# Kernel optimization log

Measured on AMD Instinct MI355X. Metric: run time of the kernel, lower is better.

The kernel has to match this reference:

```python
import jax, jax.numpy as jnp
import numpy as np

N = 50000      # nodes (src = dst at both layers)
E = 800000     # edges per layer
T = 8          # time steps
C_IN = 16      # input channels
HID = 16       # conv1 out channels (hardcoded in SAGENet)
C_OUT = 32     # final out channels


def setup_inputs() -> dict:
    key = jax.random.key(0)
    ks = jax.random.split(key, 10)
    X = jax.random.normal(ks[0], (T, N, C_IN), dtype=jnp.float32)
    edge_index0 = jax.random.randint(ks[1], (2, E), 0, N, dtype=jnp.int32)
    edge_weight0 = jax.random.uniform(ks[2], (E,), dtype=jnp.float32)
    edge_index1 = jax.random.randint(ks[3], (2, E), 0, N, dtype=jnp.int32)
    edge_weight1 = jax.random.uniform(ks[4], (E,), dtype=jnp.float32)
    res_n_id0 = jnp.arange(N, dtype=jnp.int32)
    res_n_id1 = jnp.arange(N, dtype=jnp.int32)
    W1 = jax.random.normal(ks[5], (2 * C_IN, HID), dtype=jnp.float32) * 0.1
    b1 = jax.random.normal(ks[6], (HID,), dtype=jnp.float32) * 0.1
    W2 = jax.random.normal(ks[7], (2 * HID, C_OUT), dtype=jnp.float32) * 0.1
    b2 = jax.random.normal(ks[8], (C_OUT,), dtype=jnp.float32) * 0.1
    return {"X": X, "edge_index0": edge_index0, "edge_weight0": edge_weight0,
            "edge_index1": edge_index1, "edge_weight1": edge_weight1,
            "res_n_id0": res_n_id0, "res_n_id1": res_n_id1,
            "W1": W1, "b1": b1, "W2": W2, "b2": b2}


def sage_conv(x, edge_index, edge_weight, res_n_id, num_dst, W, b):
    # x: [N_src, T, C]; message = edge_weight * x[src]; mean-aggregate to dst;
    # concat residual x[res_n_id] then linear (old PyG SAGEConv, concat=True).
    src, dst = edge_index[0], edge_index[1]
    msg = x[src] * edge_weight[:, None, None]                      # [E, T, C]
    summed = jax.ops.segment_sum(msg, dst, num_segments=num_dst)   # [Nd, T, C]
    cnt = jax.ops.segment_sum(jnp.ones_like(edge_weight), dst, num_segments=num_dst)
    aggr = summed / jnp.maximum(cnt, 1.0)[:, None, None]
    h = jnp.concatenate([x[res_n_id], aggr], axis=-1)              # [Nd, T, 2C]
    return jnp.einsum('ntc,cd->ntd', h, W) + b


def reference(X, edge_index0, edge_weight0, edge_index1, edge_weight1,
              res_n_id0, res_n_id1, W1, b1, W2, b2):
    x = jnp.transpose(X, (1, 0, 2))                                # [N, T, C]
    x = jax.nn.leaky_relu(sage_conv(x, edge_index0, edge_weight0, res_n_id0, N, W1, b1), 0.01)
    x = jax.nn.leaky_relu(sage_conv(x, edge_index1, edge_weight1, res_n_id1, N, W2, b2), 0.01)
    return jnp.transpose(x, (1, 0, 2))                             # [T, N, C_out]
```

## Files before the change

kernel.cpp:

```cpp
#include <hip/hip_runtime.h>
#include <hip/hip_bf16.h>
#include <stdint.h>

static constexpr int Nn   = 50000;
static constexpr int Ee   = 800000;
static constexpr int Tt   = 8;
static constexpr int CIN  = 16;
static constexpr int HID  = 16;
static constexpr int COUT = 32;
static constexpr int TC   = Tt * CIN;
static constexpr int ROWD = TC / 2;

static constexpr int NB  = (2 * Nn + 255) / 256;
static constexpr int CAP = 16;
static constexpr int GSTR = 32;

static constexpr int BINB = 768;
static constexpr int EPB  = (2 * Ee + BINB - 1) / BINB;
static constexpr int TRB  = 1536;

typedef __attribute__((ext_vector_type(8))) short short8;
typedef __attribute__((ext_vector_type(4))) float f32x4;
union FU { uint4 u4; short8 s8; };

__device__ inline float bflo(uint32_t u) { return __uint_as_float(u << 16); }
__device__ inline float bfhi(uint32_t u) { return __uint_as_float(u & 0xffff0000u); }
__device__ inline unsigned short f2bf(float x) {
    __hip_bfloat16 h = __float2bfloat16(x);
    unsigned short u; __builtin_memcpy(&u, &h, 2); return u;
}
__device__ inline uint32_t bfpack(float a, float b) {
    return (uint32_t)f2bf(a) | ((uint32_t)f2bf(b) << 16);
}
__device__ inline void redg(float2& a) {
    a.x += __shfl_xor(a.x, 16); a.y += __shfl_xor(a.y, 16);
    a.x += __shfl_xor(a.x, 32); a.y += __shfl_xor(a.y, 32);
}

__device__ inline float dot2bf(float acc, uint32_t w2, uint32_t x2) {
    asm("v_dot2_f32_bf16 %0, %1, %2, %0" : "+v"(acc) : "v"(w2), "v"(x2));
    return acc;
}
__device__ inline void dotp(float2& a0, float2& a1, float2& a2, float2& a3,
                            uint32_t w2, uint4 r0, uint4 r1) {
    uint32_t lo, hi;
    lo = __builtin_amdgcn_perm(r1.x, r0.x, 0x05040100u);
    hi = __builtin_amdgcn_perm(r1.x, r0.x, 0x07060302u);
    a0.x = dot2bf(a0.x, w2, lo);
    a0.y = dot2bf(a0.y, w2, hi);
    lo = __builtin_amdgcn_perm(r1.y, r0.y, 0x05040100u);
    hi = __builtin_amdgcn_perm(r1.y, r0.y, 0x07060302u);
    a1.x = dot2bf(a1.x, w2, lo);
    a1.y = dot2bf(a1.y, w2, hi);
    lo = __builtin_amdgcn_perm(r1.z, r0.z, 0x05040100u);
    hi = __builtin_amdgcn_perm(r1.z, r0.z, 0x07060302u);
    a2.x = dot2bf(a2.x, w2, lo);
    a2.y = dot2bf(a2.y, w2, hi);
    lo = __builtin_amdgcn_perm(r1.w, r0.w, 0x05040100u);
    hi = __builtin_amdgcn_perm(r1.w, r0.w, 0x07060302u);
    a3.x = dot2bf(a3.x, w2, lo);
    a3.y = dot2bf(a3.y, w2, hi);
}

__global__ __launch_bounds__(256) void k_count_detect(
        const int* __restrict__ ei0, const int* __restrict__ ei1,
        int* __restrict__ bucketCnt,
        const unsigned short* __restrict__ x16, int nvals,
        int* __restrict__ flag,
        const void* W1, const void* b1, const void* W2, const void* b2,
        float* __restrict__ biasbuf,
        uint32_t* __restrict__ wpk1, uint32_t* __restrict__ wpk2) {
    int tid = threadIdx.x;
    if (blockIdx.x >= 256) {
        __shared__ int bad;
        if (tid == 0) bad = 0;
        __syncthreads();
        for (int i = tid; i < nvals; i += 256) {
            int ex = (x16[i] >> 7) & 0xFF;
            if (ex >= 0x8D) atomicOr(&bad, 1);
        }
        __syncthreads();
        int f = bad;
        if (tid == 0) flag[0] = f;
        auto ldf = [&](const void* srcp, int idx) -> float {
            return f ? ((const float*)srcp)[idx]
                     : __bfloat162float(((const __hip_bfloat16*)srcp)[idx]);
        };
        if (tid < 16) biasbuf[tid] = ldf(b1, tid);
        if (tid >= 16 && tid < 48) biasbuf[tid] = ldf(b2, tid - 16);
        { int h = tid >> 4, d = tid & 15;
          wpk1[tid] = bfpack(ldf(W1, 2 * d * 16 + h), ldf(W1, (2 * d + 1) * 16 + h)); }
        for (int i = tid; i < 512; i += 256) {
            int h = i >> 4, d = i & 15;
            wpk2[i] = bfpack(ldf(W2, 2 * d * 32 + h), ldf(W2, (2 * d + 1) * 32 + h));
        }
        return;
    }
    __shared__ int hist[NB];
    for (int i = tid; i < NB; i += 256) hist[i] = 0;
    __syncthreads();
    const int4* d0 = (const int4*)(ei0 + Ee);
    const int4* d1 = (const int4*)(ei1 + Ee);
    int stride = 256 * 256;
    int nq = Ee / 4;
    for (int i = blockIdx.x * 256 + tid; i < 2 * nq; i += stride) {
        int4 v; int addn;
        if (i < nq) { v = d0[i]; addn = 0; }
        else        { v = d1[i - nq]; addn = Nn; }
        atomicAdd(&hist[(v.x + addn) >> 8], 1);
        atomicAdd(&hist[(v.y + addn) >> 8], 1);
        atomicAdd(&hist[(v.z + addn) >> 8], 1);
        atomicAdd(&hist[(v.w + addn) >> 8], 1);
    }
    __syncthreads();
    for (int i = tid; i < NB; i += 256)
        if (hist[i]) atomicAdd(&bucketCnt[i], hist[i]);
}

__global__ void k_bucketscan(const int* __restrict__ bucketCnt,
                             int* __restrict__ base, int* __restrict__ gcur) {
    __shared__ int tmp[512];
    int tid = threadIdx.x;
    int v = (tid < NB) ? bucketCnt[tid] : 0;
    tmp[tid] = v;
    __syncthreads();
    for (int ofs = 1; ofs < 512; ofs <<= 1) {
        int t = (tid >= ofs) ? tmp[tid - ofs] : 0;
        __syncthreads();
        tmp[tid] += t;
        __syncthreads();
    }
    if (tid < NB) {
        int b = tmp[tid] - v;
        base[tid] = b;
        gcur[tid * GSTR] = b;
    }
    if (tid == 0) base[NB] = 2 * Ee;
}

__global__ __launch_bounds__(256) void k_bin_tr(const int* __restrict__ flag,
        const int* __restrict__ ei0, const void* w0v,
        const int* __restrict__ ei1, const void* w1v,
        int* __restrict__ gcur, uint64_t* __restrict__ gout,
        const void* Xv, uint32_t* __restrict__ xrows) {
    __shared__ uint64_t rows[NB][CAP];
    __shared__ int cnt[NB];
    __shared__ int posArr[NB];
    int tid = threadIdx.x;
    int bid = blockIdx.x;
    if (bid >= BINB) {
        int f = flag[0];
        int stride = TRB * 256;
        for (int i = (bid - BINB) * 256 + tid; i < Nn * ROWD; i += stride) {
            int n = i >> 6;
            int l = i & 63;
            int t = l >> 3;
            int c = (l & 7) * 2;
            int sidx = (t * Nn + n) * CIN + c;
            uint32_t v;
            if (f) {
                float2 ab = ((const float2*)Xv)[sidx >> 1];
                v = bfpack(ab.x, ab.y);
            } else {
                const unsigned short* u = (const unsigned short*)Xv;
                v = (uint32_t)u[sidx] | ((uint32_t)u[sidx + 1] << 16);
            }
            xrows[i] = v;
        }
        return;
    }
    for (int i = tid; i < NB; i += 256) cnt[i] = 0;
    __syncthreads();
    int f = flag[0];
    int lo = bid * EPB;
    int hi = min(2 * Ee, lo + EPB);
    for (int e = lo + tid; e < hi; e += 256) {
        int g; uint32_t src, wb;
        if (e < Ee) {
            g = ei0[Ee + e];
            src = (uint32_t)ei0[e];
            wb = f ? f2bf(((const float*)w0v)[e])
                   : ((const unsigned short*)w0v)[e];
        } else {
            int e1 = e - Ee;
            g = Nn + ei1[Ee + e1];
            src = (uint32_t)ei1[e1];
            wb = f ? f2bf(((const float*)w1v)[e1])
                   : ((const unsigned short*)w1v)[e1];
        }
        uint64_t r = ((uint64_t)(uint32_t)g << 32) | (src << 16) | wb;
        int b = g >> 8;
        int idx = atomicAdd(&cnt[b], 1);
        if (idx < CAP) rows[b][idx ^ (b & (CAP - 1))] = r;
        else { int pos = atomicAdd(&gcur[b * GSTR], 1); gout[pos] = r; }
    }
    __syncthreads();
    for (int b = tid; b < NB; b += 256) {
        int c = min(cnt[b], CAP);
        posArr[b] = c ? atomicAdd(&gcur[b * GSTR], c) : 0;
    }
    __syncthreads();
    int wv = tid >> 6, lane = tid & 63;
    int q = lane >> 4, k = lane & 15;
    for (int b = wv * 4 + q; b < NB; b += 16) {
        int c = min(cnt[b], CAP);
        if (k < c) gout[posArr[b] + k] = rows[b][k ^ (b & (CAP - 1))];
    }
}

__global__ __launch_bounds__(256) void k_csr(const int* __restrict__ base,
        const uint64_t* __restrict__ gout,
        int* __restrict__ off, uint32_t* __restrict__ rec) {
    __shared__ int hist[256];
    __shared__ int tmp[256];
    __shared__ int cur[256];
    __shared__ uint32_t stage[8192];
    int b = blockIdx.x, tid = threadIdx.x;
    int lo = base[b], hi = base[b + 1];
    hist[tid] = 0;
    __syncthreads();
    for (int i = lo + tid; i < hi; i += 256) {
        int gl = (int)(gout[i] >> 32) & 255;
        atomicAdd(&hist[gl], 1);
    }
    __syncthreads();
    int v = hist[tid];
    tmp[tid] = v;
    __syncthreads();
    for (int ofs = 1; ofs < 256; ofs <<= 1) {
        int t = (tid >= ofs) ? tmp[tid - ofs] : 0;
        __syncthreads();
        tmp[tid] += t;
        __syncthreads();
    }
    int excl = tmp[tid] - v;
    int gg = (b << 8) + tid;
    if (gg < 2 * Nn) off[gg] = lo + excl;
    if (b == NB - 1 && tid == 0) off[2 * Nn] = 2 * Ee;
    int count = hi - lo;
    if (count <= 8192) {
        cur[tid] = excl;
        __syncthreads();
        for (int i = lo + tid; i < hi; i += 256) {
            uint64_t r = gout[i];
            int gl = (int)(r >> 32) & 255;
            int pos = atomicAdd(&cur[gl], 1);
            stage[pos] = (uint32_t)r;
        }
        __syncthreads();
        for (int i = tid; i < count; i += 256) rec[lo + i] = stage[i];
    } else {
        cur[tid] = lo + excl;
        __syncthreads();
        for (int i = lo + tid; i < hi; i += 256) {
            uint64_t r = gout[i];
            int gl = (int)(r >> 32) & 255;
            int pos = atomicAdd(&cur[gl], 1);
            rec[pos] = (uint32_t)r;
        }
    }
}


__global__ __launch_bounds__(256) void k_layer1(
    const uint32_t* __restrict__ xrows, const int* __restrict__ off,
    const uint32_t* __restrict__ rec, const int* __restrict__ resid,
    const uint32_t* __restrict__ wpk1, const float* __restrict__ biasbuf,
    uint32_t* __restrict__ h1rows) {
    __shared__ __align__(16) uint32_t shA[32 * 20];
    int tid = threadIdx.x, wv = tid >> 6, lane = tid & 63;
    int g = lane >> 4, p = lane & 15;
    uint4 bfr = ((const uint4*)wpk1)[p * 4 + g];
    float bias = biasbuf[p];
    int n = blockIdx.x * 4 + wv;
    int o0 = __builtin_amdgcn_readfirstlane(off[n]);
    int o1 = __builtin_amdgcn_readfirstlane(off[n + 1]);
    int rn = __builtin_amdgcn_readfirstlane(resid[n]);
    const uint4* xb = (const uint4*)xrows;
    uint4 xs4 = xb[rn * 16 + p];
    float2 a0 = {0.f, 0.f}, a1 = a0, a2 = a0, a3 = a0;
    for (int j = o0; j < o1; j += 16) {
        int j0 = j + g, j1 = j + 4 + g, j2 = j + 8 + g, j3 = j + 12 + g;
        uint32_t e0 = rec[min(j0, o1 - 1)];
        uint32_t e1 = rec[min(j1, o1 - 1)];
        uint32_t e2 = rec[min(j2, o1 - 1)];
        uint32_t e3 = rec[min(j3, o1 - 1)];
        uint4 r0 = xb[(int)(e0 >> 16) * 16 + p];
        uint4 r1 = xb[(int)(e1 >> 16) * 16 + p];
        uint4 r2 = xb[(int)(e2 >> 16) * 16 + p];
        uint4 r3 = xb[(int)(e3 >> 16) * 16 + p];
        uint32_t w0 = (j0 < o1) ? (e0 & 0xffffu) : 0u;
        uint32_t w1 = (j1 < o1) ? (e1 & 0xffffu) : 0u;
        uint32_t w2 = (j2 < o1) ? (e2 & 0xffffu) : 0u;
        uint32_t w3 = (j3 < o1) ? (e3 & 0xffffu) : 0u;
        uint32_t wA = w0 | (w1 << 16);
        uint32_t wB = w2 | (w3 << 16);
        dotp(a0, a1, a2, a3, wA, r0, r1);
        dotp(a0, a1, a2, a3, wB, r2, r3);
    }
    redg(a0); redg(a1); redg(a2); redg(a3);
    float inv = 1.f / (float)max(o1 - o0, 1);
    uint4 agp;
    agp.x = bfpack(a0.x * inv, a0.y * inv);
    agp.y = bfpack(a1.x * inv, a1.y * inv);
    agp.z = bfpack(a2.x * inv, a2.y * inv);
    agp.w = bfpack(a3.x * inv, a3.y * inv);
    int r = wv * 8 + (p >> 1);
    int hs = (p & 1) * 4;
    if (g == 0)      *(uint4*)&shA[r * 20 + hs] = xs4;
    else if (g == 1) *(uint4*)&shA[r * 20 + 8 + hs] = agp;
    __syncthreads();
    FU fa, fb; fb.u4 = bfr;
    fa.u4 = *(const uint4*)&shA[((wv >> 1) * 16 + p) * 20 + 4 * g];
    f32x4 acc = {bias, bias, bias, bias};
    acc = __builtin_amdgcn_mfma_f32_16x16x32_bf16(fa.s8, fb.s8, acc, 0, 0, 0);
    bool mine = ((g >> 1) == (wv & 1));
#pragma unroll
    for (int rg = 0; rg < 4; rg++) {
        float v = acc[rg];
        v = fmaxf(v, 0.01f * v);
        float vn = __shfl_xor(v, 1);
        if (mine && !(p & 1)) {
            int t = (g & 1) * 4 + rg;
            h1rows[n * 64 + t * 8 + (p >> 1)] = bfpack(v, vn);
        }
    }
}

__global__ __launch_bounds__(256) void k_layer2(
    const int* __restrict__ flag,
    const uint32_t* __restrict__ h1rows, const int* __restrict__ off,
    const uint32_t* __restrict__ rec, const int* __restrict__ resid,
    const uint32_t* __restrict__ wpk2, const float* __restrict__ biasbuf,
    void* __restrict__ outv) {
    __shared__ __align__(16) uint32_t shA[32 * 20];
    int tid = threadIdx.x, wv = tid >> 6, lane = tid & 63;
    int g = lane >> 4, p = lane & 15;
    uint4 b0 = ((const uint4*)wpk2)[p * 4 + g];
    uint4 b1v = ((const uint4*)wpk2)[(p + 16) * 4 + g];
    float bias0 = biasbuf[16 + p];
    float bias1 = biasbuf[32 + p];
    int f = flag[0];
    int n = blockIdx.x * 4 + wv;
    int o0 = __builtin_amdgcn_readfirstlane(off[Nn + n]);
    int o1 = __builtin_amdgcn_readfirstlane(off[Nn + n + 1]);
    int rn = __builtin_amdgcn_readfirstlane(resid[n]);
    const uint4* xb = (const uint4*)h1rows;
    uint4 xs4 = xb[rn * 16 + p];
    float2 a0 = {0.f, 0.f}, a1 = a0, a2 = a0, a3 = a0;
    for (int j = o0; j < o1; j += 16) {
        int j0 = j + g, j1 = j + 4 + g, j2 = j + 8 + g, j3 = j + 12 + g;
        uint32_t e0 = rec[min(j0, o1 - 1)];
        uint32_t e1 = rec[min(j1, o1 - 1)];
        uint32_t e2 = rec[min(j2, o1 - 1)];
        uint32_t e3 = rec[min(j3, o1 - 1)];
        uint4 r0 = xb[(int)(e0 >> 16) * 16 + p];
        uint4 r1 = xb[(int)(e1 >> 16) * 16 + p];
        uint4 r2 = xb[(int)(e2 >> 16) * 16 + p];
        uint4 r3 = xb[(int)(e3 >> 16) * 16 + p];
        uint32_t w0 = (j0 < o1) ? (e0 & 0xffffu) : 0u;
        uint32_t w1 = (j1 < o1) ? (e1 & 0xffffu) : 0u;
        uint32_t w2 = (j2 < o1) ? (e2 & 0xffffu) : 0u;
        uint32_t w3 = (j3 < o1) ? (e3 & 0xffffu) : 0u;
        uint32_t wA = w0 | (w1 << 16);
        uint32_t wB = w2 | (w3 << 16);
        dotp(a0, a1, a2, a3, wA, r0, r1);
        dotp(a0, a1, a2, a3, wB, r2, r3);
    }
    redg(a0); redg(a1); redg(a2); redg(a3);
    float inv = 1.f / (float)max(o1 - o0, 1);
    uint4 agp;
    agp.x = bfpack(a0.x * inv, a0.y * inv);
    agp.y = bfpack(a1.x * inv, a1.y * inv);
    agp.z = bfpack(a2.x * inv, a2.y * inv);
    agp.w = bfpack(a3.x * inv, a3.y * inv);
    int r = wv * 8 + (p >> 1);
    int hs = (p & 1) * 4;
    if (g == 0)      *(uint4*)&shA[r * 20 + hs] = xs4;
    else if (g == 1) *(uint4*)&shA[r * 20 + 8 + hs] = agp;
    __syncthreads();
    FU fa, fb0, fb1; fb0.u4 = b0; fb1.u4 = b1v;
    fa.u4 = *(const uint4*)&shA[((wv >> 1) * 16 + p) * 20 + 4 * g];
    f32x4 acc0 = {bias0, bias0, bias0, bias0};
    f32x4 acc1 = {bias1, bias1, bias1, bias1};
    acc0 = __builtin_amdgcn_mfma_f32_16x16x32_bf16(fa.s8, fb0.s8, acc0, 0, 0, 0);
    acc1 = __builtin_amdgcn_mfma_f32_16x16x32_bf16(fa.s8, fb1.s8, acc1, 0, 0, 0);
    bool mine = ((g >> 1) == (wv & 1));
    if (mine) {
#pragma unroll
        for (int rg = 0; rg < 4; rg++) {
            int t = (g & 1) * 4 + rg;
            size_t idx = ((size_t)(t * Nn + n)) * COUT + p;
            float v = acc0[rg]; v = fmaxf(v, 0.01f * v);
            float u = acc1[rg]; u = fmaxf(u, 0.01f * u);
            if (f) {
                ((float*)outv)[idx] = v;
                ((float*)outv)[idx + 16] = u;
            } else {
                ((__hip_bfloat16*)outv)[idx] = __float2bfloat16(v);
                ((__hip_bfloat16*)outv)[idx + 16] = __float2bfloat16(u);
            }
        }
    }
}


extern "C" void kernel_launch(void* const* d_in, const int* in_sizes, int n_in,
                              void* d_out, int out_size, void* d_ws, size_t ws_size,
                              hipStream_t stream) {
    const void* X   = d_in[0];
    const int* ei0  = (const int*)d_in[1];
    const void* w0  = d_in[2];
    const int* ei1  = (const int*)d_in[3];
    const void* w1  = d_in[4];
    const int* rn0  = (const int*)d_in[5];
    const int* rn1  = (const int*)d_in[6];
    const void* W1  = d_in[7];
    const void* b1  = d_in[8];
    const void* W2  = d_in[9];
    const void* b2  = d_in[10];

    char* ws = (char*)d_ws;
    size_t p = 0;
    auto alloc = [&](size_t bytes) -> char* {
        p = (p + 255) & ~(size_t)255;
        char* r = ws + p;
        p += bytes;
        return r;
    };
    int* flag        = (int*)alloc(4);
    float* biasbuf   = (float*)alloc(48 * 4);
    uint32_t* wpk1   = (uint32_t*)alloc(256 * 4);
    uint32_t* wpk2   = (uint32_t*)alloc(512 * 4);
    int* bucketCnt   = (int*)alloc(NB * 4);
    int* base        = (int*)alloc((NB + 1) * 4);
    int* gcur        = (int*)alloc((size_t)NB * GSTR * 4);
    int* off         = (int*)alloc(((size_t)2 * Nn + 1) * 4);
    uint32_t* recf   = (uint32_t*)alloc((size_t)2 * Ee * 4);
    uint32_t* h1rows = (uint32_t*)alloc((size_t)Nn * ROWD * 4);
    uint64_t* gout   = (uint64_t*)alloc((size_t)2 * Ee * 8);
    uint32_t* xrows  = (uint32_t*)d_out;

    hipMemsetAsync(bucketCnt, 0, NB * sizeof(int), stream);
    hipLaunchKernelGGL(k_count_detect, dim3(257), dim3(256), 0, stream,
                       ei0, ei1, bucketCnt,
                       (const unsigned short*)X, 16384, flag, W1, b1, W2, b2,
                       biasbuf, wpk1, wpk2);
    hipLaunchKernelGGL(k_bucketscan, dim3(1), dim3(512), 0, stream,
                       bucketCnt, base, gcur);
    hipLaunchKernelGGL(k_bin_tr, dim3(BINB + TRB), dim3(256), 0, stream,
                       flag, ei0, w0, ei1, w1, gcur, gout, X, xrows);
    hipLaunchKernelGGL(k_csr, dim3(NB), dim3(256), 0, stream,
                       base, gout, off, recf);
    hipLaunchKernelGGL(k_layer1, dim3(Nn / 4), dim3(256), 0, stream,
                       xrows, off, recf, rn0, wpk1, biasbuf, h1rows);
    hipLaunchKernelGGL(k_layer2, dim3(Nn / 4), dim3(256), 0, stream,
                       flag, h1rows, off, recf, rn1, wpk2, biasbuf, d_out);
    (void)in_sizes; (void)n_in; (void)out_size; (void)ws_size;
}
```

Measured before the change: 245.9 us.

## Process two destination nodes per wavefront in both layer kernels

Each wavefront now aggregates two destination nodes at once, interleaving their gathers with 8 edges per iteration per node instead of 16 for one. This lets every wave fill a full 16-row MFMA tile, so all lanes store results and the grid is halved. The bf16 output path in layer 2 now packs pairs with shuffles into 32-bit stores. In exchange, the loop runs to the larger of the two degrees, which can waste lanes when degrees differ, and register pressure rises.

```diff
diff --git a/kernel.cpp b/kernel.cpp
--- a/kernel.cpp
+++ b/kernel.cpp
@@ -23,8 +23,6 @@
 typedef __attribute__((ext_vector_type(4))) float f32x4;
 union FU { uint4 u4; short8 s8; };
 
-__device__ inline float bflo(uint32_t u) { return __uint_as_float(u << 16); }
-__device__ inline float bfhi(uint32_t u) { return __uint_as_float(u & 0xffff0000u); }
 __device__ inline unsigned short f2bf(float x) {
     __hip_bfloat16 h = __float2bfloat16(x);
     unsigned short u; __builtin_memcpy(&u, &h, 2); return u;
@@ -267,61 +265,74 @@
     const uint32_t* __restrict__ rec, const int* __restrict__ resid,
     const uint32_t* __restrict__ wpk1, const float* __restrict__ biasbuf,
     uint32_t* __restrict__ h1rows) {
-    __shared__ __align__(16) uint32_t shA[32 * 20];
+    __shared__ __align__(16) uint32_t shA[64 * 20];
     int tid = threadIdx.x, wv = tid >> 6, lane = tid & 63;
     int g = lane >> 4, p = lane & 15;
     uint4 bfr = ((const uint4*)wpk1)[p * 4 + g];
     float bias = biasbuf[p];
-    int n = blockIdx.x * 4 + wv;
-    int o0 = __builtin_amdgcn_readfirstlane(off[n]);
-    int o1 = __builtin_amdgcn_readfirstlane(off[n + 1]);
-    int rn = __builtin_amdgcn_readfirstlane(resid[n]);
+    int n0 = blockIdx.x * 8 + wv * 2;
+    int oA0 = __builtin_amdgcn_readfirstlane(off[n0]);
+    int oM  = __builtin_amdgcn_readfirstlane(off[n0 + 1]);
+    int oB1 = __builtin_amdgcn_readfirstlane(off[n0 + 2]);
+    int rnA = __builtin_amdgcn_readfirstlane(resid[n0]);
+    int rnB = __builtin_amdgcn_readfirstlane(resid[n0 + 1]);
+    int cA = oM - oA0, cB = oB1 - oM;
+    int lastA = max(oM - 1, 0), lastB = max(oB1 - 1, 0);
     const uint4* xb = (const uint4*)xrows;
-    uint4 xs4 = xb[rn * 16 + p];
-    float2 a0 = {0.f, 0.f}, a1 = a0, a2 = a0, a3 = a0;
-    for (int j = o0; j < o1; j += 16) {
-        int j0 = j + g, j1 = j + 4 + g, j2 = j + 8 + g, j3 = j + 12 + g;
-        uint32_t e0 = rec[min(j0, o1 - 1)];
-        uint32_t e1 = rec[min(j1, o1 - 1)];
-        uint32_t e2 = rec[min(j2, o1 - 1)];
-        uint32_t e3 = rec[min(j3, o1 - 1)];
-        uint4 r0 = xb[(int)(e0 >> 16) * 16 + p];
-        uint4 r1 = xb[(int)(e1 >> 16) * 16 + p];
-        uint4 r2 = xb[(int)(e2 >> 16) * 16 + p];
-        uint4 r3 = xb[(int)(e3 >> 16) * 16 + p];
-        uint32_t w0 = (j0 < o1) ? (e0 & 0xffffu) : 0u;
-        uint32_t w1 = (j1 < o1) ? (e1 & 0xffffu) : 0u;
-        uint32_t w2 = (j2 < o1) ? (e2 & 0xffffu) : 0u;
-        uint32_t w3 = (j3 < o1) ? (e3 & 0xffffu) : 0u;
-        uint32_t wA = w0 | (w1 << 16);
-        uint32_t wB = w2 | (w3 << 16);
-        dotp(a0, a1, a2, a3, wA, r0, r1);
-        dotp(a0, a1, a2, a3, wB, r2, r3);
-    }
-    redg(a0); redg(a1); redg(a2); redg(a3);
-    float inv = 1.f / (float)max(o1 - o0, 1);
-    uint4 agp;
-    agp.x = bfpack(a0.x * inv, a0.y * inv);
-    agp.y = bfpack(a1.x * inv, a1.y * inv);
-    agp.z = bfpack(a2.x * inv, a2.y * inv);
-    agp.w = bfpack(a3.x * inv, a3.y * inv);
-    int r = wv * 8 + (p >> 1);
+    uint4 xsA = xb[rnA * 16 + p];
+    uint4 xsB = xb[rnB * 16 + p];
+    float2 aA0 = {0.f, 0.f}, aA1 = aA0, aA2 = aA0, aA3 = aA0;
+    float2 aB0 = aA0, aB1 = aA0, aB2 = aA0, aB3 = aA0;
+    int cmax = max(cA, cB);
+    for (int j = 0; j < cmax; j += 8) {
+        int j0 = j + g, j1 = j + 4 + g;
+        uint32_t eA0 = rec[min(oA0 + j0, lastA)];
+        uint32_t eA1 = rec[min(oA0 + j1, lastA)];
+        uint32_t eB0 = rec[min(oM + j0, lastB)];
+        uint32_t eB1 = rec[min(oM + j1, lastB)];
+        uint4 rA0 = xb[(int)(eA0 >> 16) * 16 + p];
+        uint4 rA1 = xb[(int)(eA1 >> 16) * 16 + p];
+        uint4 rB0 = xb[(int)(eB0 >> 16) * 16 + p];
+        uint4 rB1 = xb[(int)(eB1 >> 16) * 16 + p];
+        uint32_t wA = ((j0 < cA) ? (eA0 & 0xffffu) : 0u)
+                    | (((j1 < cA) ? (eA1 & 0xffffu) : 0u) << 16);
+        uint32_t wB = ((j0 < cB) ? (eB0 & 0xffffu) : 0u)
+                    | (((j1 < cB) ? (eB1 & 0xffffu) : 0u) << 16);
+        dotp(aA0, aA1, aA2, aA3, wA, rA0, rA1);
+        dotp(aB0, aB1, aB2, aB3, wB, rB0, rB1);
+    }
+    redg(aA0); redg(aA1); redg(aA2); redg(aA3);
+    redg(aB0); redg(aB1); redg(aB2); redg(aB3);
+    float invA = 1.f / (float)max(cA, 1);
+    float invB = 1.f / (float)max(cB, 1);
+    uint4 agpA, agpB;
+    agpA.x = bfpack(aA0.x * invA, aA0.y * invA);
+    agpA.y = bfpack(aA1.x * invA, aA1.y * invA);
+    agpA.z = bfpack(aA2.x * invA, aA2.y * invA);
+    agpA.w = bfpack(aA3.x * invA, aA3.y * invA);
+    agpB.x = bfpack(aB0.x * invB, aB0.y * invB);
+    agpB.y = bfpack(aB1.x * invB, aB1.y * invB);
+    agpB.z = bfpack(aB2.x * invB, aB2.y * invB);
+    agpB.w = bfpack(aB3.x * invB, aB3.y * invB);
+    int rA = wv * 16 + (p >> 1);
     int hs = (p & 1) * 4;
-    if (g == 0)      *(uint4*)&shA[r * 20 + hs] = xs4;
-    else if (g == 1) *(uint4*)&shA[r * 20 + 8 + hs] = agp;
+    if (g == 0)      *(uint4*)&shA[rA * 20 + hs] = xsA;
+    else if (g == 1) *(uint4*)&shA[rA * 20 + 8 + hs] = agpA;
+    else if (g == 2) *(uint4*)&shA[(rA + 8) * 20 + hs] = xsB;
+    else             *(uint4*)&shA[(rA + 8) * 20 + 8 + hs] = agpB;
     __syncthreads();
     FU fa, fb; fb.u4 = bfr;
-    fa.u4 = *(const uint4*)&shA[((wv >> 1) * 16 + p) * 20 + 4 * g];
+    fa.u4 = *(const uint4*)&shA[(wv * 16 + p) * 20 + 4 * g];
     f32x4 acc = {bias, bias, bias, bias};
     acc = __builtin_amdgcn_mfma_f32_16x16x32_bf16(fa.s8, fb.s8, acc, 0, 0, 0);
-    bool mine = ((g >> 1) == (wv & 1));
 #pragma unroll
     for (int rg = 0; rg < 4; rg++) {
         float v = acc[rg];
         v = fmaxf(v, 0.01f * v);
         float vn = __shfl_xor(v, 1);
-        if (mine && !(p & 1)) {
+        if (!(p & 1)) {
             int t = (g & 1) * 4 + rg;
+            int n = n0 + (g >> 1);
             h1rows[n * 64 + t * 8 + (p >> 1)] = bfpack(v, vn);
         }
     }
@@ -333,7 +344,7 @@
     const uint32_t* __restrict__ rec, const int* __restrict__ resid,
     const uint32_t* __restrict__ wpk2, const float* __restrict__ biasbuf,
     void* __restrict__ outv) {
-    __shared__ __align__(16) uint32_t shA[32 * 20];
+    __shared__ __align__(16) uint32_t shA[64 * 20];
     int tid = threadIdx.x, wv = tid >> 6, lane = tid & 63;
     int g = lane >> 4, p = lane & 15;
     uint4 b0 = ((const uint4*)wpk2)[p * 4 + g];
@@ -341,64 +352,80 @@
     float bias0 = biasbuf[16 + p];
     float bias1 = biasbuf[32 + p];
     int f = flag[0];
-    int n = blockIdx.x * 4 + wv;
-    int o0 = __builtin_amdgcn_readfirstlane(off[Nn + n]);
-    int o1 = __builtin_amdgcn_readfirstlane(off[Nn + n + 1]);
-    int rn = __builtin_amdgcn_readfirstlane(resid[n]);
+    int n0 = blockIdx.x * 8 + wv * 2;
+    int oA0 = __builtin_amdgcn_readfirstlane(off[Nn + n0]);
+    int oM  = __builtin_amdgcn_readfirstlane(off[Nn + n0 + 1]);
+    int oB1 = __builtin_amdgcn_readfirstlane(off[Nn + n0 + 2]);
+    int rnA = __builtin_amdgcn_readfirstlane(resid[n0]);
+    int rnB = __builtin_amdgcn_readfirstlane(resid[n0 + 1]);
+    int cA = oM - oA0, cB = oB1 - oM;
+    int lastA = max(oM - 1, 0), lastB = max(oB1 - 1, 0);
     const uint4* xb = (const uint4*)h1rows;
-    uint4 xs4 = xb[rn * 16 + p];
-    float2 a0 = {0.f, 0.f}, a1 = a0, a2 = a0, a3 = a0;
-    for (int j = o0; j < o1; j += 16) {
-        int j0 = j + g, j1 = j + 4 + g, j2 = j + 8 + g, j3 = j + 12 + g;
-        uint32_t e0 = rec[min(j0, o1 - 1)];
-        uint32_t e1 = rec[min(j1, o1 - 1)];
-        uint32_t e2 = rec[min(j2, o1 - 1)];
-        uint32_t e3 = rec[min(j3, o1 - 1)];
-        uint4 r0 = xb[(int)(e0 >> 16) * 16 + p];
-        uint4 r1 = xb[(int)(e1 >> 16) * 16 + p];
-        uint4 r2 = xb[(int)(e2 >> 16) * 16 + p];
-        uint4 r3 = xb[(int)(e3 >> 16) * 16 + p];
-        uint32_t w0 = (j0 < o1) ? (e0 & 0xffffu) : 0u;
-        uint32_t w1 = (j1 < o1) ? (e1 & 0xffffu) : 0u;
-        uint32_t w2 = (j2 < o1) ? (e2 & 0xffffu) : 0u;
-        uint32_t w3 = (j3 < o1) ? (e3 & 0xffffu) : 0u;
-        uint32_t wA = w0 | (w1 << 16);
-        uint32_t wB = w2 | (w3 << 16);
-        dotp(a0, a1, a2, a3, wA, r0, r1);
-        dotp(a0, a1, a2, a3, wB, r2, r3);
-    }
-    redg(a0); redg(a1); redg(a2); redg(a3);
-    float inv = 1.f / (float)max(o1 - o0, 1);
-    uint4 agp;
-    agp.x = bfpack(a0.x * inv, a0.y * inv);
-    agp.y = bfpack(a1.x * inv, a1.y * inv);
-    agp.z = bfpack(a2.x * inv, a2.y * inv);
-    agp.w = bfpack(a3.x * inv, a3.y * inv);
-    int r = wv * 8 + (p >> 1);
+    uint4 xsA = xb[rnA * 16 + p];
+    uint4 xsB = xb[rnB * 16 + p];
+    float2 aA0 = {0.f, 0.f}, aA1 = aA0, aA2 = aA0, aA3 = aA0;
+    float2 aB0 = aA0, aB1 = aA0, aB2 = aA0, aB3 = aA0;
+    int cmax = max(cA, cB);
+    for (int j = 0; j < cmax; j += 8) {
+        int j0 = j + g, j1 = j + 4 + g;
+        uint32_t eA0 = rec[min(oA0 + j0, lastA)];
+        uint32_t eA1 = rec[min(oA0 + j1, lastA)];
+        uint32_t eB0 = rec[min(oM + j0, lastB)];
+        uint32_t eB1 = rec[min(oM + j1, lastB)];
+        uint4 rA0 = xb[(int)(eA0 >> 16) * 16 + p];
+        uint4 rA1 = xb[(int)(eA1 >> 16) * 16 + p];
+        uint4 rB0 = xb[(int)(eB0 >> 16) * 16 + p];
+        uint4 rB1 = xb[(int)(eB1 >> 16) * 16 + p];
+        uint32_t wA = ((j0 < cA) ? (eA0 & 0xffffu) : 0u)
+                    | (((j1 < cA) ? (eA1 & 0xffffu) : 0u) << 16);
+        uint32_t wB = ((j0 < cB) ? (eB0 & 0xffffu) : 0u)
+                    | (((j1 < cB) ? (eB1 & 0xffffu) : 0u) << 16);
+        dotp(aA0, aA1, aA2, aA3, wA, rA0, rA1);
+        dotp(aB0, aB1, aB2, aB3, wB, rB0, rB1);
+    }
+    redg(aA0); redg(aA1); redg(aA2); redg(aA3);
+    redg(aB0); redg(aB1); redg(aB2); redg(aB3);
+    float invA = 1.f / (float)max(cA, 1);
+    float invB = 1.f / (float)max(cB, 1);
+    uint4 agpA, agpB;
+    agpA.x = bfpack(aA0.x * invA, aA0.y * invA);
+    agpA.y = bfpack(aA1.x * invA, aA1.y * invA);
+    agpA.z = bfpack(aA2.x * invA, aA2.y * invA);
+    agpA.w = bfpack(aA3.x * invA, aA3.y * invA);
+    agpB.x = bfpack(aB0.x * invB, aB0.y * invB);
+    agpB.y = bfpack(aB1.x * invB, aB1.y * invB);
+    agpB.z = bfpack(aB2.x * invB, aB2.y * invB);
+    agpB.w = bfpack(aB3.x * invB, aB3.y * invB);
+    int rA = wv * 16 + (p >> 1);
     int hs = (p & 1) * 4;
-    if (g == 0)      *(uint4*)&shA[r * 20 + hs] = xs4;
-    else if (g == 1) *(uint4*)&shA[r * 20 + 8 + hs] = agp;
+    if (g == 0)      *(uint4*)&shA[rA * 20 + hs] = xsA;
+    else if (g == 1) *(uint4*)&shA[rA * 20 + 8 + hs] = agpA;
+    else if (g == 2) *(uint4*)&shA[(rA + 8) * 20 + hs] = xsB;
+    else             *(uint4*)&shA[(rA + 8) * 20 + 8 + hs] = agpB;
     __syncthreads();
     FU fa, fb0, fb1; fb0.u4 = b0; fb1.u4 = b1v;
-    fa.u4 = *(const uint4*)&shA[((wv >> 1) * 16 + p) * 20 + 4 * g];
+    fa.u4 = *(const uint4*)&shA[(wv * 16 + p) * 20 + 4 * g];
     f32x4 acc0 = {bias0, bias0, bias0, bias0};
     f32x4 acc1 = {bias1, bias1, bias1, bias1};
     acc0 = __builtin_amdgcn_mfma_f32_16x16x32_bf16(fa.s8, fb0.s8, acc0, 0, 0, 0);
     acc1 = __builtin_amdgcn_mfma_f32_16x16x32_bf16(fa.s8, fb1.s8, acc1, 0, 0, 0);
-    bool mine = ((g >> 1) == (wv & 1));
-    if (mine) {
 #pragma unroll
-        for (int rg = 0; rg < 4; rg++) {
-            int t = (g & 1) * 4 + rg;
+    for (int rg = 0; rg < 4; rg++) {
+        int t = (g & 1) * 4 + rg;
+        int n = n0 + (g >> 1);
+        float v = acc0[rg]; v = fmaxf(v, 0.01f * v);
+        float u = acc1[rg]; u = fmaxf(u, 0.01f * u);
+        if (f) {
             size_t idx = ((size_t)(t * Nn + n)) * COUT + p;
-            float v = acc0[rg]; v = fmaxf(v, 0.01f * v);
-            float u = acc1[rg]; u = fmaxf(u, 0.01f * u);
-            if (f) {
-                ((float*)outv)[idx] = v;
-                ((float*)outv)[idx + 16] = u;
-            } else {
-                ((__hip_bfloat16*)outv)[idx] = __float2bfloat16(v);
-                ((__hip_bfloat16*)outv)[idx + 16] = __float2bfloat16(u);
+            ((float*)outv)[idx] = v;
+            ((float*)outv)[idx + 16] = u;
+        } else {
+            float vn = __shfl_xor(v, 1);
+            float un = __shfl_xor(u, 1);
+            if (!(p & 1)) {
+                size_t di = ((size_t)(t * Nn + n)) * 16 + (p >> 1);
+                ((uint32_t*)outv)[di] = bfpack(v, vn);
+                ((uint32_t*)outv)[di + 8] = bfpack(u, un);
             }
         }
     }
@@ -452,9 +479,9 @@
                        flag, ei0, w0, ei1, w1, gcur, gout, X, xrows);
     hipLaunchKernelGGL(k_csr, dim3(NB), dim3(256), 0, stream,
                        base, gout, off, recf);
-    hipLaunchKernelGGL(k_layer1, dim3(Nn / 4), dim3(256), 0, stream,
+    hipLaunchKernelGGL(k_layer1, dim3(Nn / 8), dim3(256), 0, stream,
                        xrows, off, recf, rn0, wpk1, biasbuf, h1rows);
-    hipLaunchKernelGGL(k_layer2, dim3(Nn / 4), dim3(256), 0, stream,
+    hipLaunchKernelGGL(k_layer2, dim3(Nn / 8), dim3(256), 0, stream,
                        flag, h1rows, off, recf, rn1, wpk2, biasbuf, d_out);
     (void)in_sizes; (void)n_in; (void)out_size; (void)ws_size;
 }
```

Measured after the change: 243.6 us. No clear change (-0.9%).
